# Kernel tuning notes

Hardware: AMD Instinct MI355X
Metric: run time of the kernel (lower is better)

Reference implementation:

```python
import jax, jax.numpy as jnp
import numpy as np

IN_SIZE, HIDDEN, N_STEPS = 512, 1024, 5
B, L = 32, 1024

def setup_inputs():
    key = jax.random.key(0)
    ks = jax.random.split(key, 11)
    s = 1.0 / np.sqrt(HIDDEN).astype(np.float32)
    u = lambda k, shape: jax.random.uniform(k, shape, jnp.float32, -s, s)
    return {
        "x": jax.random.normal(ks[0], (B, L, IN_SIZE), jnp.float32),
        "w_ih": u(ks[1], (3 * HIDDEN, IN_SIZE)),   # torch GRU weight_ih_l0 (gate order r,z,n)
        "w_hh": u(ks[2], (3 * HIDDEN, HIDDEN)),    # unused math-wise (h0=0) but kept for faithfulness
        "b_ih": u(ks[3], (3 * HIDDEN,)),
        "b_hh": u(ks[4], (3 * HIDDEN,)),
        "WH": u(ks[5], (N_STEPS, HIDDEN, HIDDEN)),
        "bH": u(ks[6], (N_STEPS, HIDDEN)),
        "WT": u(ks[7], (N_STEPS, HIDDEN, HIDDEN)),
        "bT": u(ks[8], (N_STEPS, HIDDEN)),
        "WC": u(ks[9], (N_STEPS, HIDDEN, HIDDEN)),
        "bC": u(ks[10], (N_STEPS, HIDDEN)),
    }

def reference(x, w_ih, w_hh, b_ih, b_hh, WH, bH, WT, bT, WC, bC):
    # Single-timestep GRU (seq_len==1 after view(-1, L, F)), h0 = 0.
    gi = jnp.einsum("blf,gf->blg", x, w_ih) + b_ih            # [B, L, 3H]
    i_r, i_z, i_n = jnp.split(gi, 3, axis=-1)
    b_hr, b_hz, b_hn = jnp.split(b_hh, 3)
    # w_hh @ h0 == 0; only the hidden biases survive.
    r = jax.nn.sigmoid(i_r + b_hr)
    z = jax.nn.sigmoid(i_z + b_hz)
    n = jnp.tanh(i_n + r * b_hn)
    h = (1.0 - z) * n                                          # h' = (1-z)*n + z*0
    # keep w_hh in the graph with zero contribution (faithful param set)
    h = h + 0.0 * jnp.sum(w_hh) * jnp.zeros_like(h[..., :1])

    def micro(h, params):
        wh, bh, wt, bt, wc, bc = params
        hh = jnp.tanh(jnp.einsum("blh,oh->blo", h, wh) + bh)
        t = jax.nn.sigmoid(jnp.einsum("blh,oh->blo", h, wt) + bt)
        c = jax.nn.sigmoid(jnp.einsum("blh,oh->blo", h, wc) + bc)
        return hh * t + h * (1.0 - c), None

    h, _ = jax.lax.scan(micro, h, (WH, bH, WT, bT, WC, bC))
    return h  # [B, L, HIDDEN], == torch.cat over batch items
```

## Files before the change

### kernel.cpp

```cpp
#include <hip/hip_runtime.h>
#include <math.h>

#define MROWS 32768
#define MH    16384
#define HID   1024
#define KGRU  512

typedef float          f32x4  __attribute__((ext_vector_type(4)));
typedef short          bf16x8 __attribute__((ext_vector_type(8)));
typedef unsigned short u16x4  __attribute__((ext_vector_type(4)));

__device__ __forceinline__ float sigm(float x) { return 1.0f / (1.0f + expf(-x)); }

__device__ __forceinline__ unsigned short f2bf(float f) {
    union { float f; unsigned u; } v; v.f = f;
    unsigned r = v.u + 0x7FFFu + ((v.u >> 16) & 1u);
    return (unsigned short)(r >> 16);
}

__device__ __forceinline__ void gld16(const void* g, void* l) {
    __builtin_amdgcn_global_load_lds((const __attribute__((address_space(1))) void*)g,
                                     (__attribute__((address_space(3))) void*)l, 16, 0, 0);
}

template <int K, bool IS_GRU>
__global__ __launch_bounds__(256, 2) void gemm3(
    const unsigned short* __restrict__ Abf,
    const unsigned short* __restrict__ W0,
    const float* __restrict__ b0, const float* __restrict__ b1, const float* __restrict__ b2,
    const float* __restrict__ bhh,
    float* __restrict__ outF,
    unsigned short* __restrict__ outBf)
{
    __shared__ short Al[16 * 512];
    __shared__ short Wl[24 * 512];

    const int tid  = threadIdx.x;
    const int lane = tid & 63;
    const int wid  = tid >> 6;
    const int wm   = wid >> 1;
    const int wn   = wid & 1;
    const int l15  = lane & 15;
    const int l4   = lane >> 4;

    const int nwg   = gridDim.x;
    const int cpx   = nwg >> 3;
    const int wg    = blockIdx.x;
    const int swz   = (wg & 7) * cpx + (wg >> 3);
    const int m0    = (swz >> 4) * 128;
    const int n0    = (swz & 15) * 64;

    long aoff[4];
#pragma unroll
    for (int i = 0; i < 4; i++) {
        const int ca = wid * 4 + i;
        const int f = ca >> 1, ks = ca & 1;
        aoff[i] = (long)(m0 + f * 16 + l15) * K + ks * 32 + l4 * 8;
    }
    long woff[6];
#pragma unroll
    for (int i = 0; i < 6; i++) {
        const int cw = wid * 6 + i;
        const int q = cw >> 3, nf = (cw >> 1) & 3, ks = cw & 1;
        woff[i] = (long)q * HID * K + (long)(n0 + nf * 16 + l15) * K + ks * 32 + l4 * 8;
    }

    f32x4 acc[3][2][4];
#pragma unroll
    for (int q = 0; q < 3; q++)
#pragma unroll
        for (int c = 0; c < 2; c++)
#pragma unroll
            for (int f = 0; f < 4; f++) acc[q][c][f] = (f32x4)0.0f;

    for (int k0 = 0; k0 < K; k0 += 64) {
#pragma unroll
        for (int i = 0; i < 4; i++) gld16(Abf + aoff[i] + k0, Al + (wid * 4 + i) * 512);
#pragma unroll
        for (int i = 0; i < 6; i++) gld16(W0 + woff[i] + k0, Wl + (wid * 6 + i) * 512);
        __syncthreads();

#pragma unroll
        for (int ks = 0; ks < 2; ks++) {
            bf16x8 ha[4], wb[3][2];
#pragma unroll
            for (int f = 0; f < 4; f++)
                ha[f] = *(const bf16x8*)&Al[((wm * 4 + f) * 2 + ks) * 512 + lane * 8];
#pragma unroll
            for (int q = 0; q < 3; q++)
#pragma unroll
                for (int c = 0; c < 2; c++)
                    wb[q][c] = *(const bf16x8*)&Wl[(q * 8 + (wn * 2 + c) * 2 + ks) * 512 + lane * 8];
#pragma unroll
            for (int q = 0; q < 3; q++)
#pragma unroll
                for (int c = 0; c < 2; c++)
#pragma unroll
                    for (int f = 0; f < 4; f++)
                        acc[q][c][f] = __builtin_amdgcn_mfma_f32_16x16x32_bf16(
                            wb[q][c], ha[f], acc[q][c][f], 0, 0, 0);
        }
        __syncthreads();
    }

    const int gn0 = n0 + wn * 32 + l4 * 4;
    const int gn1 = gn0 + 16;
    f32x4 vb[3][2], vh[3][2];
    vb[0][0] = *(const f32x4*)&b0[gn0]; vb[0][1] = *(const f32x4*)&b0[gn1];
    vb[1][0] = *(const f32x4*)&b1[gn0]; vb[1][1] = *(const f32x4*)&b1[gn1];
    vb[2][0] = *(const f32x4*)&b2[gn0]; vb[2][1] = *(const f32x4*)&b2[gn1];
    if constexpr (IS_GRU) {
        vh[0][0] = *(const f32x4*)&bhh[gn0];           vh[0][1] = *(const f32x4*)&bhh[gn1];
        vh[1][0] = *(const f32x4*)&bhh[HID + gn0];     vh[1][1] = *(const f32x4*)&bhh[HID + gn1];
        vh[2][0] = *(const f32x4*)&bhh[2 * HID + gn0]; vh[2][1] = *(const f32x4*)&bhh[2 * HID + gn1];
    }

#pragma unroll
    for (int f = 0; f < 4; f++) {
        const long gm = m0 + wm * 64 + f * 16 + l15;
#pragma unroll
        for (int c = 0; c < 2; c++) {
            const int gn = c ? gn1 : gn0;
            const f32x4 g0 = acc[0][c][f], g1 = acc[1][c][f], g2 = acc[2][c][f];
            f32x4 res;
            if constexpr (IS_GRU) {
#pragma unroll
                for (int j = 0; j < 4; j++) {
                    float r = sigm(g0[j] + vb[0][c][j] + vh[0][c][j]);
                    float z = sigm(g1[j] + vb[1][c][j] + vh[1][c][j]);
                    float n = tanhf(g2[j] + vb[2][c][j] + r * vh[2][c][j]);
                    res[j] = (1.0f - z) * n;
                }
            } else {
                const f32x4 hold = *(const f32x4*)&outF[gm * HID + gn];
#pragma unroll
                for (int j = 0; j < 4; j++) {
                    float hh = tanhf(g0[j] + vb[0][c][j]);
                    float tt = sigm(g1[j] + vb[1][c][j]);
                    float cc = sigm(g2[j] + vb[2][c][j]);
                    res[j] = hh * tt + hold[j] * (1.0f - cc);
                }
            }
            *(f32x4*)&outF[gm * HID + gn] = res;
            u16x4 rb;
#pragma unroll
            for (int j = 0; j < 4; j++) rb[j] = f2bf(res[j]);
            *(u16x4*)&outBf[gm * HID + gn] = rb;
        }
    }
}

__global__ void convP(const float* __restrict__ s, unsigned short* __restrict__ d, int n) {
    int i = (blockIdx.x * blockDim.x + threadIdx.x) * 4;
    const int stride = gridDim.x * blockDim.x * 4;
    for (; i < n; i += stride) {
        f32x4 v = *(const f32x4*)&s[i];
        u16x4 r;
#pragma unroll
        for (int j = 0; j < 4; j++) r[j] = f2bf(v[j]);
        *(u16x4*)&d[i] = r;
    }
}

__global__ void convS(const float* __restrict__ s, unsigned short* __restrict__ d, int n) {
    int i = (blockIdx.x * blockDim.x + threadIdx.x) * 4;
    const int stride = gridDim.x * blockDim.x * 4;
    for (; i < n; i += stride) {
        f32x4 v = *(const f32x4*)&s[i];
        u16x4 r;
#pragma unroll
        for (int j = 0; j < 4; j++) r[j] = f2bf(v[j]);
        const int di = (i >> 20) * (3 * HID * HID) + (i & (HID * HID - 1));
        *(u16x4*)&d[di] = r;
    }
}

extern "C" void kernel_launch(void* const* d_in, const int* in_sizes, int n_in,
                              void* d_out, int out_size, void* d_ws, size_t ws_size,
                              hipStream_t stream) {
    const float* x    = (const float*)d_in[0];
    const float* w_ih = (const float*)d_in[1];
    const float* b_ih = (const float*)d_in[3];
    const float* b_hh = (const float*)d_in[4];
    const float* WH   = (const float*)d_in[5];
    const float* bH   = (const float*)d_in[6];
    const float* WT   = (const float*)d_in[7];
    const float* bT   = (const float*)d_in[8];
    const float* WC   = (const float*)d_in[9];
    const float* bC   = (const float*)d_in[10];

    float* out = (float*)d_out;
    char*  ws  = (char*)d_ws;

    unsigned short* wih_bf = (unsigned short*)ws;
    unsigned short* W_bf   = (unsigned short*)(ws + (size_t)3 * HID * KGRU * 2);
    const size_t off_ping  = (size_t)3 * HID * KGRU * 2 + (size_t)15 * HID * HID * 2;
    unsigned short* ping   = (unsigned short*)(ws + off_ping);
    unsigned short* pong   = (unsigned short*)(ws + off_ping + (size_t)MH * HID * 2);

    dim3 blk(256);

    convP<<<1024, blk, 0, stream>>>(w_ih, wih_bf, 3 * HID * KGRU);
    convS<<<2048, blk, 0, stream>>>(WH, W_bf + 0 * HID * HID, 5 * HID * HID);
    convS<<<2048, blk, 0, stream>>>(WT, W_bf + 1 * HID * HID, 5 * HID * HID);
    convS<<<2048, blk, 0, stream>>>(WC, W_bf + 2 * HID * HID, 5 * HID * HID);

    for (int h = 0; h < 2; h++) {
        const float* xh   = x + (size_t)h * MH * KGRU;
        float*       outh = out + (size_t)h * MH * HID;

        convP<<<2048, blk, 0, stream>>>(xh, pong, MH * KGRU);

        gemm3<KGRU, true><<<2048, blk, 0, stream>>>(
            pong, wih_bf, b_ih, b_ih + HID, b_ih + 2 * HID, b_hh, outh, ping);

        const unsigned short* src = ping;
        for (int s = 0; s < 5; s++) {
            unsigned short* dst = (s & 1) ? ping : pong;
            gemm3<HID, false><<<2048, blk, 0, stream>>>(
                src, W_bf + (size_t)s * 3 * HID * HID,
                bH + s * HID, bT + s * HID, bC + s * HID, nullptr, outh, dst);
            src = dst;
        }
    }
}
```

Before: 2.131 ms.

## Double-buffer LDS tiles in gemm3 and prefetch residual state before main loop

The K loop now keeps two LDS stages, so the async global-to-LDS load of the next 64-wide K tile is issued before MFMA compute on the current tile. This removes one barrier per tile and hides load latency behind compute. The fp32 residual h used in the highway epilogue is also loaded into registers before the main loop instead of in the epilogue. LDS use doubles to 80KB per block and 32 extra VGPRs stay live through the loop, which may reduce occupancy below the two blocks per CU requested by launch bounds.

```diff
diff --git a/kernel.cpp b/kernel.cpp
--- a/kernel.cpp
+++ b/kernel.cpp
@@ -32,8 +32,7 @@
     float* __restrict__ outF,
     unsigned short* __restrict__ outBf)
 {
-    __shared__ short Al[16 * 512];
-    __shared__ short Wl[24 * 512];
+    __shared__ short L[2][40 * 512];
 
     const int tid  = threadIdx.x;
     const int lane = tid & 63;
@@ -43,12 +42,12 @@
     const int l15  = lane & 15;
     const int l4   = lane >> 4;
 
-    const int nwg   = gridDim.x;
-    const int cpx   = nwg >> 3;
-    const int wg    = blockIdx.x;
-    const int swz   = (wg & 7) * cpx + (wg >> 3);
-    const int m0    = (swz >> 4) * 128;
-    const int n0    = (swz & 15) * 64;
+    const int nwg = gridDim.x;
+    const int cpx = nwg >> 3;
+    const int wg  = blockIdx.x;
+    const int swz = (wg & 7) * cpx + (wg >> 3);
+    const int m0  = (swz >> 4) * 128;
+    const int n0  = (swz & 15) * 64;
 
     long aoff[4];
 #pragma unroll
@@ -65,6 +64,18 @@
         woff[i] = (long)q * HID * K + (long)(n0 + nf * 16 + l15) * K + ks * 32 + l4 * 8;
     }
 
+    const int gn0 = n0 + wn * 32 + l4 * 4;
+    f32x4 hold[4][2];
+    if constexpr (!IS_GRU) {
+#pragma unroll
+        for (int f = 0; f < 4; f++) {
+            const long gm = m0 + wm * 64 + f * 16 + l15;
+#pragma unroll
+            for (int c = 0; c < 2; c++)
+                hold[f][c] = *(const f32x4*)&outF[gm * HID + gn0 + c * 16];
+        }
+    }
+
     f32x4 acc[3][2][4];
 #pragma unroll
     for (int q = 0; q < 3; q++)
@@ -73,24 +84,24 @@
 #pragma unroll
             for (int f = 0; f < 4; f++) acc[q][c][f] = (f32x4)0.0f;
 
-    for (int k0 = 0; k0 < K; k0 += 64) {
-#pragma unroll
-        for (int i = 0; i < 4; i++) gld16(Abf + aoff[i] + k0, Al + (wid * 4 + i) * 512);
-#pragma unroll
-        for (int i = 0; i < 6; i++) gld16(W0 + woff[i] + k0, Wl + (wid * 6 + i) * 512);
-        __syncthreads();
-
+    auto stage = [&](short* Lw, int k0) {
+#pragma unroll
+        for (int i = 0; i < 4; i++) gld16(Abf + aoff[i] + k0, Lw + (wid * 4 + i) * 512);
+#pragma unroll
+        for (int i = 0; i < 6; i++) gld16(W0 + woff[i] + k0, Lw + (16 + wid * 6 + i) * 512);
+    };
+    auto compute = [&](const short* Lr) {
 #pragma unroll
         for (int ks = 0; ks < 2; ks++) {
             bf16x8 ha[4], wb[3][2];
 #pragma unroll
             for (int f = 0; f < 4; f++)
-                ha[f] = *(const bf16x8*)&Al[((wm * 4 + f) * 2 + ks) * 512 + lane * 8];
+                ha[f] = *(const bf16x8*)&Lr[((wm * 4 + f) * 2 + ks) * 512 + lane * 8];
 #pragma unroll
             for (int q = 0; q < 3; q++)
 #pragma unroll
                 for (int c = 0; c < 2; c++)
-                    wb[q][c] = *(const bf16x8*)&Wl[(q * 8 + (wn * 2 + c) * 2 + ks) * 512 + lane * 8];
+                    wb[q][c] = *(const bf16x8*)&Lr[(16 + q * 8 + (wn * 2 + c) * 2 + ks) * 512 + lane * 8];
 #pragma unroll
             for (int q = 0; q < 3; q++)
 #pragma unroll
@@ -100,10 +111,22 @@
                         acc[q][c][f] = __builtin_amdgcn_mfma_f32_16x16x32_bf16(
                             wb[q][c], ha[f], acc[q][c][f], 0, 0, 0);
         }
+    };
+
+    constexpr int NT = K / 64;
+
+    stage(L[0], 0);
+    __syncthreads();
+
+    for (int t = 0; t < NT; t += 2) {
+        stage(L[1], (t + 1) * 64);
+        compute(L[0]);
         __syncthreads();
-    }
-
-    const int gn0 = n0 + wn * 32 + l4 * 4;
+        if (t + 2 < NT) stage(L[0], (t + 2) * 64);
+        compute(L[1]);
+        __syncthreads();
+    }
+
     const int gn1 = gn0 + 16;
     f32x4 vb[3][2], vh[3][2];
     vb[0][0] = *(const f32x4*)&b0[gn0]; vb[0][1] = *(const f32x4*)&b0[gn1];
@@ -132,13 +155,12 @@
                     res[j] = (1.0f - z) * n;
                 }
             } else {
-                const f32x4 hold = *(const f32x4*)&outF[gm * HID + gn];
 #pragma unroll
                 for (int j = 0; j < 4; j++) {
                     float hh = tanhf(g0[j] + vb[0][c][j]);
                     float tt = sigm(g1[j] + vb[1][c][j]);
                     float cc = sigm(g2[j] + vb[2][c][j]);
-                    res[j] = hh * tt + hold[j] * (1.0f - cc);
+                    res[j] = hh * tt + hold[f][c][j] * (1.0f - cc);
                 }
             }
             *(f32x4*)&outF[gm * HID + gn] = res;
```

New measurement: 2.254 ms. 1.06x slower.
